# Kernel tuning notes

Measured on AMD Instinct MI355X. Metric: run time of the kernel, lower is better.

Reference implementation:

```python
import jax, jax.numpy as jnp
import numpy as np

B, CIN, COUT, K, H, W = 8, 256, 256, 3, 64, 64
STRIDE, PAD, DIL, DG = 1, 1, 1, 1
K2 = K * K


def _conv2d(x, w, b):
    out = jax.lax.conv_general_dilated(
        x, w, (STRIDE, STRIDE), [(PAD, PAD), (PAD, PAD)],
        rhs_dilation=(DIL, DIL),
        dimension_numbers=('NCHW', 'OIHW', 'NCHW'))
    return out + b[None, :, None, None]


def _deform_conv2d(x, offset, mask, weight, bias):
    # torchvision.ops.deform_conv2d semantics (DCNv2, bilinear, zero outside).
    Bn, Cin, Hin, Win = x.shape
    O = weight.shape[0]
    dg, Cg = DG, Cin // DG
    Ho, Wo = offset.shape[2], offset.shape[3]
    # offset channel layout: [dg, K2, (dy,dx)] interleaved per kernel point
    off = offset.reshape(Bn, dg, K2, 2, Ho, Wo)
    dy, dx = off[:, :, :, 0], off[:, :, :, 1]
    m = mask.reshape(Bn, dg, K2, Ho, Wo)
    ky, kx = jnp.meshgrid(jnp.arange(K), jnp.arange(K), indexing='ij')
    ky = ky.reshape(K2).astype(x.dtype)
    kx = kx.reshape(K2).astype(x.dtype)
    base_y = jnp.arange(Ho, dtype=x.dtype) * STRIDE - PAD
    base_x = jnp.arange(Wo, dtype=x.dtype) * STRIDE - PAD
    # sampling positions [B, dg, K2, Ho, Wo]
    py = base_y[None, None, None, :, None] + (ky * DIL)[None, None, :, None, None] + dy
    px = base_x[None, None, None, None, :] + (kx * DIL)[None, None, :, None, None] + dx
    y0 = jnp.floor(py)
    x0 = jnp.floor(px)
    ly, lx = py - y0, px - x0

    xflat = x.reshape(Bn, dg, Cg, Hin * Win)

    def gather_one(xg, idx):
        return jnp.take(xg, idx, axis=1)

    gather = jax.vmap(jax.vmap(gather_one))  # over B, dg

    def corner(yc, xc, wgt):
        valid = (yc >= 0) & (yc <= Hin - 1) & (xc >= 0) & (xc <= Win - 1)
        yi = jnp.clip(yc, 0, Hin - 1).astype(jnp.int32)
        xi = jnp.clip(xc, 0, Win - 1).astype(jnp.int32)
        idx = (yi * Win + xi).reshape(Bn, dg, K2 * Ho * Wo)
        v = gather(xflat, idx).reshape(Bn, dg, Cg, K2, Ho, Wo)
        w = jnp.where(valid, wgt, jnp.zeros_like(wgt))
        return v * w[:, :, None]  # broadcast over Cg

    sampled = (corner(y0, x0, (1 - ly) * (1 - lx))
               + corner(y0, x0 + 1, (1 - ly) * lx)
               + corner(y0 + 1, x0, ly * (1 - lx))
               + corner(y0 + 1, x0 + 1, ly * lx))
    sampled = sampled * m[:, :, None]  # modulation mask
    wk = weight.reshape(O, dg, Cg, K2)
    out = jnp.einsum('ogck,bgckhw->bohw', wk, sampled)
    return out + bias[None, :, None, None]


def reference(x, weight, bias, w_off, b_off):
    om = _conv2d(x, w_off, b_off)  # [B, 3*dg*K2, H, W]
    n = DG * K2
    o1, o2, mask = om[:, :n], om[:, n:2 * n], om[:, 2 * n:]
    offset = jnp.concatenate([o1, o2], axis=1)
    mask = jax.nn.sigmoid(mask)
    return _deform_conv2d(x, offset, mask, weight, bias)


def setup_inputs():
    key = jax.random.key(0)
    k1, k2, k3, k4, k5 = jax.random.split(key, 5)
    fan_in = CIN * K2
    bound = 1.0 / np.sqrt(fan_in).astype(np.float32)
    x = jax.random.normal(k1, (B, CIN, H, W), dtype=jnp.float32)
    weight = jax.random.uniform(k2, (COUT, CIN, K, K), minval=-bound, maxval=bound, dtype=jnp.float32)
    bias = jax.random.uniform(k3, (COUT,), minval=-bound, maxval=bound, dtype=jnp.float32)
    # small random offset-conv params (zero init in the source is degenerate)
    w_off = jax.random.normal(k4, (3 * K2 * DG, CIN, K, K), dtype=jnp.float32) * 0.01
    b_off = jax.random.normal(k5, (3 * K2 * DG,), dtype=jnp.float32) * 0.01
    return {"x": x, "weight": weight, "bias": bias, "w_off": w_off, "b_off": b_off}
```

## Files before the change

### kernel.cpp

```cpp
#include <hip/hip_runtime.h>
#include <hip/hip_bf16.h>
#include <stdint.h>

typedef short bf16x8 __attribute__((ext_vector_type(8)));
typedef float f32x4  __attribute__((ext_vector_type(4)));

#define NB   8
#define NC   256
#define NO   256
#define HH   64
#define WW   64
#define NPIX 4096
#define KTOT 2304
#define NKC  72

#define XN_OFF  0u
#define XN_SZ   (NB*NPIX*NC*2u)
#define WP_OFF  (XN_OFF + XN_SZ)
#define WP_SZ   (KTOT*NO*2u)
#define WPO_OFF (WP_OFF + WP_SZ)
#define WPO_SZ  (KTOT*32u*2u)
#define OM_OFF  (WPO_OFF + WPO_SZ)
#define OM_SZ   (NB*NPIX*32u*4u)
#define PY_OFF  (OM_OFF + OM_SZ)
#define CO_SZ   (NB*9u*NPIX*4u)
#define PX_OFF  (PY_OFF + CO_SZ)
#define MK_OFF  (PX_OFF + CO_SZ)

__device__ __forceinline__ float b2f(short s) {
    union { unsigned u; float f; } z; z.u = ((unsigned)(unsigned short)s) << 16; return z.f;
}
__device__ __forceinline__ short f2b(float f) {
    __hip_bfloat16 h = __float2bfloat16(f);
    short s; __builtin_memcpy(&s, &h, 2); return s;
}

__global__ void pack_x(const float* __restrict__ x, unsigned short* __restrict__ xn) {
    __shared__ float tile[64][65];
    int blk = blockIdx.x;
    int pt = blk & 63, ct = (blk >> 6) & 3, b = blk >> 8;
    int t = threadIdx.x;
    int pi = t & 63, ci0 = t >> 6;
    const float* src = x + ((size_t)(b*NC + ct*64))*NPIX + (size_t)pt*64;
#pragma unroll
    for (int j = 0; j < 16; ++j)
        tile[ci0 + 4*j][pi] = src[(size_t)(ci0 + 4*j)*NPIX + pi];
    __syncthreads();
    int c = t & 63, pj0 = t >> 6;
    unsigned short* dst = xn + ((size_t)b*NPIX + (size_t)pt*64)*NC + ct*64;
#pragma unroll
    for (int j = 0; j < 16; ++j) {
        int pj = pj0 + 4*j;
        dst[(size_t)pj*NC + c] = (unsigned short)f2b(tile[c][pj]);
    }
}

__global__ void pack_w(const float* __restrict__ weight, unsigned short* __restrict__ wp) {
    int idx = blockIdx.x*256 + threadIdx.x;
    int e = idx & 7, l = (idx >> 3) & 63, nt = (idx >> 9) & 15, kc = idx >> 13;
    int k  = kc*32 + 8*(l >> 4) + e;
    int k2 = k >> 8, c = k & 255;
    int ky = k2 / 3, kx = k2 - 3*ky;
    int o  = nt*16 + (l & 15);
    float v = weight[(size_t)(o*NC + c)*9 + ky*3 + kx];
    wp[idx] = (unsigned short)f2b(v);
}

__global__ void pack_wo(const float* __restrict__ w_off, unsigned short* __restrict__ wpo) {
    int idx = blockIdx.x*256 + threadIdx.x;
    int e = idx & 7, l = (idx >> 3) & 63, nt = (idx >> 9) & 1, kc = idx >> 10;
    int k  = kc*32 + 8*(l >> 4) + e;
    int k2 = k >> 8, c = k & 255;
    int ky = k2 / 3, kx = k2 - 3*ky;
    int n  = nt*16 + (l & 15);
    float v = (n < 27) ? w_off[(size_t)(n*NC + c)*9 + ky*3 + kx] : 0.0f;
    wpo[idx] = (unsigned short)f2b(v);
}

__launch_bounds__(256, 2)
__global__ void off_conv(const unsigned short* __restrict__ xn,
                         const unsigned short* __restrict__ wpo,
                         float* __restrict__ om) {
    int bid = blockIdx.x;
    int lid = (bid & 7)*64 + (bid >> 3);
    int mt = lid & 63, b = lid >> 6;
    int t = threadIdx.x, wv = t >> 6, l = t & 63, g = l >> 4;
    int pix = mt*64 + wv*16 + (l & 15);
    int y = pix >> 6, xx = pix & 63;
    f32x4 acc0 = {0.f,0.f,0.f,0.f}, acc1 = {0.f,0.f,0.f,0.f};
    const char* xc = (const char*)(xn + (size_t)b*NPIX*NC);
    const bf16x8* wpf = (const bf16x8*)wpo;
    const bf16x8 zero8 = {0,0,0,0,0,0,0,0};

    auto aaddr = [&](int kc)->const char* {
        int k2 = kc >> 3, cc = kc & 7;
        int ky = k2 / 3, kx = k2 - 3*ky;
        int sy = y + ky - 1, sx = xx + kx - 1;
        int cs = min(max(sy,0),HH-1)*WW + min(max(sx,0),WW-1);
        return xc + ((size_t)cs*NC + cc*32 + g*8)*2;
    };
    auto avalid = [&](int kc)->bool {
        int k2 = kc >> 3;
        int ky = k2 / 3, kx = k2 - 3*ky;
        int sy = y + ky - 1, sx = xx + kx - 1;
        return (sy>=0)&(sy<HH)&(sx>=0)&(sx<WW);
    };

    bf16x8 a_c = *(const bf16x8*)aaddr(0);
    bf16x8 w0c = wpf[l], w1c = wpf[64 + l];
    bool v_c = avalid(0);
#pragma unroll
    for (int kc = 0; kc < NKC; ++kc) {
        int kn = (kc < NKC-1) ? kc+1 : kc;
        bf16x8 a_n = *(const bf16x8*)aaddr(kn);
        bf16x8 w0n = wpf[(size_t)(kn*2)*64 + l];
        bf16x8 w1n = wpf[(size_t)(kn*2+1)*64 + l];
        bool v_n = avalid(kn);
        bf16x8 au = v_c ? a_c : zero8;
        acc0 = __builtin_amdgcn_mfma_f32_16x16x32_bf16(au, w0c, acc0, 0, 0, 0);
        acc1 = __builtin_amdgcn_mfma_f32_16x16x32_bf16(au, w1c, acc1, 0, 0, 0);
        a_c = a_n; w0c = w0n; w1c = w1n; v_c = v_n;
    }
#pragma unroll
    for (int r = 0; r < 4; ++r) {
        int pm = mt*64 + wv*16 + 4*g + r;
        om[((size_t)b*NPIX + pm)*32 +      (l & 15)] = acc0[r];
        om[((size_t)b*NPIX + pm)*32 + 16 + (l & 15)] = acc1[r];
    }
}

__global__ void coords_k(const float* __restrict__ om, const float* __restrict__ b_off,
                         float* __restrict__ py, float* __restrict__ px,
                         float* __restrict__ mk) {
    int idx = blockIdx.x*256 + threadIdx.x;
    if (idx >= NB*9*NPIX) return;
    int pix = idx & 4095;
    int k   = (idx >> 12) % 9;
    int b   = idx / (9*NPIX);
    const float* omp = om + ((size_t)b*NPIX + pix)*32;
    float dy = omp[2*k]     + b_off[2*k];
    float dx = omp[2*k + 1] + b_off[2*k + 1];
    float m  = omp[18 + k]  + b_off[18 + k];
    float yy = (float)(pix >> 6) - 1.0f + (float)(k / 3) + dy;
    float xv = (float)(pix & 63) - 1.0f + (float)(k % 3) + dx;
    py[idx] = yy;
    px[idx] = xv;
    mk[idx] = 1.0f / (1.0f + __expf(-m));
}

__launch_bounds__(256, 2)
__global__ void dcn_main(const unsigned short* __restrict__ xn,
                         const unsigned short* __restrict__ wpack,
                         const float* __restrict__ pyA,
                         const float* __restrict__ pxA,
                         const float* __restrict__ mkA,
                         const float* __restrict__ bias,
                         float* __restrict__ out) {
    __shared__ unsigned short lds[2][4096];
    int bid = blockIdx.x;
    int lid = (bid & 7)*64 + (bid >> 3);
    int nh  = lid & 1;
    int mtg = lid >> 1;
    int mt = mtg & 31, b = mtg >> 5;
    int t = threadIdx.x, wv = t >> 6, l = t & 63, g = l >> 4;
    int pix0 = mt*128 + wv*32 + (l & 15);

    f32x4 acc[2][8];
#pragma unroll
    for (int f = 0; f < 2; ++f)
#pragma unroll
        for (int nt = 0; nt < 8; ++nt) acc[f][nt] = f32x4{0.f,0.f,0.f,0.f};

    const char* xc = (const char*)(xn + (size_t)b*NPIX*NC);
    const unsigned short* wpb = wpack + nh*4096 + wv*1024 + l*8;

    float cw[2][4];  const char* bp[2][4];
    float ncw[2][4]; const char* nbp[2][4];
    float npy[2], npx[2], nm[2];

    auto coord_compute = [&](float py, float px, float m, float* cwf, const char** bpf) {
        float y0f = floorf(py), x0f = floorf(px);
        float ly = py - y0f, lx = px - x0f;
        int iy0 = (int)y0f, ix0 = (int)x0f;
        int iy1 = iy0 + 1,  ix1 = ix0 + 1;
        bool vy0 = (iy0 >= 0) & (iy0 < HH);
        bool vy1 = (iy1 >= 0) & (iy1 < HH);
        bool vx0 = (ix0 >= 0) & (ix0 < WW);
        bool vx1 = (ix1 >= 0) & (ix1 < WW);
        float wy0 = (1.f - ly) * m, wy1 = ly * m;
        cwf[0] = (vy0 & vx0) ? wy0 * (1.f - lx) : 0.f;
        cwf[1] = (vy0 & vx1) ? wy0 * lx         : 0.f;
        cwf[2] = (vy1 & vx0) ? wy1 * (1.f - lx) : 0.f;
        cwf[3] = (vy1 & vx1) ? wy1 * lx         : 0.f;
        int cy0 = min(max(iy0,0),HH-1), cy1 = min(max(iy1,0),HH-1);
        int cx0 = min(max(ix0,0),WW-1), cx1 = min(max(ix1,0),WW-1);
        bpf[0] = xc + ((size_t)(cy0*WW + cx0)*NC + g*8)*2;
        bpf[1] = xc + ((size_t)(cy0*WW + cx1)*NC + g*8)*2;
        bpf[2] = xc + ((size_t)(cy1*WW + cx0)*NC + g*8)*2;
        bpf[3] = xc + ((size_t)(cy1*WW + cx1)*NC + g*8)*2;
    };

#define STAGEW(bi, kcs) do {                                                           \
        const unsigned short* _gs = wpb + (size_t)(kcs)*8192;                          \
        _Pragma("unroll")                                                              \
        for (int _i = 0; _i < 2; ++_i) {                                               \
            __builtin_amdgcn_global_load_lds(                                          \
                (const __attribute__((address_space(1))) unsigned int*)(_gs + _i*512), \
                (__attribute__((address_space(3))) unsigned int*)(&lds[bi][wv*1024 + _i*512]), \
                16, 0, 0);                                                             \
        }                                                                              \
    } while (0)

#pragma unroll
    for (int f = 0; f < 2; ++f) {
        int ci = ((b*9) << 12) + pix0 + f*16;
        coord_compute(pyA[ci], pxA[ci], mkA[ci], cw[f], bp[f]);
    }
    bf16x8 cur[2][4], nxt[2][4];
#pragma unroll
    for (int f = 0; f < 2; ++f)
#pragma unroll
        for (int c = 0; c < 4; ++c)
            cur[f][c] = *(const bf16x8*)bp[f][c];
    STAGEW(0, 0);
    __syncthreads();

    for (int k2 = 0; k2 < 9; ++k2) {
        int k2n = (k2 < 8) ? k2 + 1 : 8;
#pragma unroll
        for (int cc = 0; cc < 8; ++cc) {
            int kc = k2*8 + cc;
            if (kc < NKC-1) STAGEW((kc+1) & 1, kc+1);
            if (cc == 2) {
#pragma unroll
                for (int f = 0; f < 2; ++f) {
                    int ci = ((b*9 + k2n) << 12) + pix0 + f*16;
                    npy[f] = pyA[ci]; npx[f] = pxA[ci]; nm[f] = mkA[ci];
                }
            }
            if (cc == 5) {
#pragma unroll
                for (int f = 0; f < 2; ++f)
                    coord_compute(npy[f], npx[f], nm[f], ncw[f], nbp[f]);
            }
#pragma unroll
            for (int f = 0; f < 2; ++f)
#pragma unroll
                for (int c = 0; c < 4; ++c)
                    nxt[f][c] = (cc < 7) ? *(const bf16x8*)(bp[f][c] + (cc+1)*64)
                                         : *(const bf16x8*)(nbp[f][c]);
            bf16x8 af[2];
#pragma unroll
            for (int f = 0; f < 2; ++f) {
#pragma unroll
                for (int e = 0; e < 8; ++e) {
                    float v = cw[f][0]*b2f(cur[f][0][e]) + cw[f][1]*b2f(cur[f][1][e])
                            + cw[f][2]*b2f(cur[f][2][e]) + cw[f][3]*b2f(cur[f][3][e]);
                    af[f][e] = f2b(v);
                }
            }
            const bf16x8* bl = (const bf16x8*)&lds[kc & 1][0];
#pragma unroll
            for (int nt = 0; nt < 8; ++nt) {
                bf16x8 wf = bl[nt*64 + l];
                acc[0][nt] = __builtin_amdgcn_mfma_f32_16x16x32_bf16(af[0], wf, acc[0][nt], 0, 0, 0);
                acc[1][nt] = __builtin_amdgcn_mfma_f32_16x16x32_bf16(af[1], wf, acc[1][nt], 0, 0, 0);
            }
            __syncthreads();
#pragma unroll
            for (int f = 0; f < 2; ++f)
#pragma unroll
                for (int c = 0; c < 4; ++c)
                    cur[f][c] = nxt[f][c];
            if (cc == 7) {
#pragma unroll
                for (int f = 0; f < 2; ++f)
#pragma unroll
                    for (int c = 0; c < 4; ++c) { cw[f][c] = ncw[f][c]; bp[f][c] = nbp[f][c]; }
            }
        }
    }
#undef STAGEW

#pragma unroll
    for (int f = 0; f < 2; ++f)
#pragma unroll
        for (int nt = 0; nt < 8; ++nt) {
            int o = nh*128 + nt*16 + (l & 15);
            float bv = bias[o];
            f32x4 r = acc[f][nt] + bv;
            *(f32x4*)(out + ((size_t)(b*NO + o))*NPIX + (mt*128 + wv*32 + f*16 + 4*g)) = r;
        }
}

extern "C" void kernel_launch(void* const* d_in, const int* in_sizes, int n_in,
                              void* d_out, int out_size, void* d_ws, size_t ws_size,
                              hipStream_t stream) {
    const float* x      = (const float*)d_in[0];
    const float* weight = (const float*)d_in[1];
    const float* bias   = (const float*)d_in[2];
    const float* w_off  = (const float*)d_in[3];
    const float* b_off  = (const float*)d_in[4];
    float* out = (float*)d_out;
    char* ws = (char*)d_ws;

    unsigned short* xn  = (unsigned short*)(ws + XN_OFF);
    unsigned short* wp  = (unsigned short*)(ws + WP_OFF);
    unsigned short* wpo = (unsigned short*)(ws + WPO_OFF);
    float* om = (float*)(ws + OM_OFF);
    float* py = (float*)(ws + PY_OFF);
    float* px = (float*)(ws + PX_OFF);
    float* mk = (float*)(ws + MK_OFF);

    pack_x  <<<2048, 256, 0, stream>>>(x, xn);
    pack_w  <<<KTOT*NO/256,  256, 0, stream>>>(weight, wp);
    pack_wo <<<KTOT*32/256,  256, 0, stream>>>(w_off, wpo);
    off_conv<<<512, 256, 0, stream>>>(xn, wpo, om);
    coords_k<<<NB*9*NPIX/256, 256, 0, stream>>>(om, b_off, py, px, mk);
    dcn_main<<<512, 256, 0, stream>>>(xn, wp, py, px, mk, bias, out);
}
```

Baseline: 265.5 us.

## Vectorize pack_x, deepen off_conv prefetch, triple-buffer dcn_main with smaller tiles

pack_x now uses 16-byte vector loads and stores instead of scalar accesses. off_conv moves to 128-thread blocks with a three-stage register prefetch. dcn_main halves its per-block pixel tile and doubles the grid. It adds a third LDS weight buffer and replaces the per-step __syncthreads with explicit vmcnt waits and raw barriers, aiming to overlap global loads with MFMA work and raise occupancy. The hand-tuned waitcnt counts are fragile and could race if the compiler reorders loads, and smaller tiles reduce weight reuse per block.

```diff
diff --git a/kernel.cpp b/kernel.cpp
--- a/kernel.cpp
+++ b/kernel.cpp
@@ -40,18 +40,26 @@
     int blk = blockIdx.x;
     int pt = blk & 63, ct = (blk >> 6) & 3, b = blk >> 8;
     int t = threadIdx.x;
-    int pi = t & 63, ci0 = t >> 6;
+    int ci = t >> 4, p4 = (t & 15) * 4;
     const float* src = x + ((size_t)(b*NC + ct*64))*NPIX + (size_t)pt*64;
 #pragma unroll
-    for (int j = 0; j < 16; ++j)
-        tile[ci0 + 4*j][pi] = src[(size_t)(ci0 + 4*j)*NPIX + pi];
+    for (int j = 0; j < 4; ++j) {
+        f32x4 v = *(const f32x4*)(src + (size_t)(ci + 16*j)*NPIX + p4);
+        tile[ci + 16*j][p4+0] = v[0];
+        tile[ci + 16*j][p4+1] = v[1];
+        tile[ci + 16*j][p4+2] = v[2];
+        tile[ci + 16*j][p4+3] = v[3];
+    }
     __syncthreads();
-    int c = t & 63, pj0 = t >> 6;
-    unsigned short* dst = xn + ((size_t)b*NPIX + (size_t)pt*64)*NC + ct*64;
-#pragma unroll
-    for (int j = 0; j < 16; ++j) {
-        int pj = pj0 + 4*j;
-        dst[(size_t)pj*NC + c] = (unsigned short)f2b(tile[c][pj]);
+    int c8 = (t & 7) * 8, pj0 = t >> 3;
+    unsigned short* dst = xn + ((size_t)b*NPIX + (size_t)pt*64)*NC + ct*64 + c8;
+#pragma unroll
+    for (int j = 0; j < 2; ++j) {
+        int pj = pj0 + 32*j;
+        bf16x8 o;
+#pragma unroll
+        for (int e = 0; e < 8; ++e) o[e] = f2b(tile[c8 + e][pj]);
+        *(bf16x8*)(dst + (size_t)pj*NC) = o;
     }
 }
 
@@ -77,15 +85,14 @@
     wpo[idx] = (unsigned short)f2b(v);
 }
 
-__launch_bounds__(256, 2)
+__launch_bounds__(128, 4)
 __global__ void off_conv(const unsigned short* __restrict__ xn,
                          const unsigned short* __restrict__ wpo,
                          float* __restrict__ om) {
     int bid = blockIdx.x;
-    int lid = (bid & 7)*64 + (bid >> 3);
-    int mt = lid & 63, b = lid >> 6;
+    int b = bid & 7, mt = bid >> 3;
     int t = threadIdx.x, wv = t >> 6, l = t & 63, g = l >> 4;
-    int pix = mt*64 + wv*16 + (l & 15);
+    int pix = mt*32 + wv*16 + (l & 15);
     int y = pix >> 6, xx = pix & 63;
     f32x4 acc0 = {0.f,0.f,0.f,0.f}, acc1 = {0.f,0.f,0.f,0.f};
     const char* xc = (const char*)(xn + (size_t)b*NPIX*NC);
@@ -106,24 +113,32 @@
         return (sy>=0)&(sy<HH)&(sx>=0)&(sx<WW);
     };
 
-    bf16x8 a_c = *(const bf16x8*)aaddr(0);
-    bf16x8 w0c = wpf[l], w1c = wpf[64 + l];
-    bool v_c = avalid(0);
+    bf16x8 a[3], w0[3], w1[3];
+    bool v[3];
+#pragma unroll
+    for (int s = 0; s < 3; ++s) {
+        a[s]  = *(const bf16x8*)aaddr(s);
+        w0[s] = wpf[(size_t)(s*2)*64 + l];
+        w1[s] = wpf[(size_t)(s*2+1)*64 + l];
+        v[s]  = avalid(s);
+    }
 #pragma unroll
     for (int kc = 0; kc < NKC; ++kc) {
-        int kn = (kc < NKC-1) ? kc+1 : kc;
-        bf16x8 a_n = *(const bf16x8*)aaddr(kn);
-        bf16x8 w0n = wpf[(size_t)(kn*2)*64 + l];
-        bf16x8 w1n = wpf[(size_t)(kn*2+1)*64 + l];
-        bool v_n = avalid(kn);
-        bf16x8 au = v_c ? a_c : zero8;
-        acc0 = __builtin_amdgcn_mfma_f32_16x16x32_bf16(au, w0c, acc0, 0, 0, 0);
-        acc1 = __builtin_amdgcn_mfma_f32_16x16x32_bf16(au, w1c, acc1, 0, 0, 0);
-        a_c = a_n; w0c = w0n; w1c = w1n; v_c = v_n;
+        int s = kc % 3;
+        bf16x8 au = v[s] ? a[s] : zero8;
+        acc0 = __builtin_amdgcn_mfma_f32_16x16x32_bf16(au, w0[s], acc0, 0, 0, 0);
+        acc1 = __builtin_amdgcn_mfma_f32_16x16x32_bf16(au, w1[s], acc1, 0, 0, 0);
+        int kp = kc + 3;
+        if (kp < NKC) {
+            a[s]  = *(const bf16x8*)aaddr(kp);
+            w0[s] = wpf[(size_t)(kp*2)*64 + l];
+            w1[s] = wpf[(size_t)(kp*2+1)*64 + l];
+            v[s]  = avalid(kp);
+        }
     }
 #pragma unroll
     for (int r = 0; r < 4; ++r) {
-        int pm = mt*64 + wv*16 + 4*g + r;
+        int pm = mt*32 + wv*16 + 4*g + r;
         om[((size_t)b*NPIX + pm)*32 +      (l & 15)] = acc0[r];
         om[((size_t)b*NPIX + pm)*32 + 16 + (l & 15)] = acc1[r];
     }
@@ -148,7 +163,7 @@
     mk[idx] = 1.0f / (1.0f + __expf(-m));
 }
 
-__launch_bounds__(256, 2)
+__launch_bounds__(256, 4)
 __global__ void dcn_main(const unsigned short* __restrict__ xn,
                          const unsigned short* __restrict__ wpack,
                          const float* __restrict__ pyA,
@@ -156,27 +171,24 @@
                          const float* __restrict__ mkA,
                          const float* __restrict__ bias,
                          float* __restrict__ out) {
-    __shared__ unsigned short lds[2][4096];
+    __shared__ unsigned short lds[3][4096];
     int bid = blockIdx.x;
-    int lid = (bid & 7)*64 + (bid >> 3);
-    int nh  = lid & 1;
-    int mtg = lid >> 1;
-    int mt = mtg & 31, b = mtg >> 5;
+    int b   = bid & 7;
+    int loc = bid >> 3;
+    int mt  = loc >> 1, nh = loc & 1;
     int t = threadIdx.x, wv = t >> 6, l = t & 63, g = l >> 4;
-    int pix0 = mt*128 + wv*32 + (l & 15);
-
-    f32x4 acc[2][8];
-#pragma unroll
-    for (int f = 0; f < 2; ++f)
-#pragma unroll
-        for (int nt = 0; nt < 8; ++nt) acc[f][nt] = f32x4{0.f,0.f,0.f,0.f};
+    int pix0 = mt*64 + wv*16 + (l & 15);
+
+    f32x4 acc[8];
+#pragma unroll
+    for (int i = 0; i < 8; ++i) acc[i] = f32x4{0.f,0.f,0.f,0.f};
 
     const char* xc = (const char*)(xn + (size_t)b*NPIX*NC);
     const unsigned short* wpb = wpack + nh*4096 + wv*1024 + l*8;
 
-    float cw[2][4];  const char* bp[2][4];
-    float ncw[2][4]; const char* nbp[2][4];
-    float npy[2], npx[2], nm[2];
+    float cw[4], ncw[4];
+    const char *bp[4], *nbp[4];
+    float npy, npx, nm;
 
     auto coord_compute = [&](float py, float px, float m, float* cwf, const char** bpf) {
         float y0f = floorf(py), x0f = floorf(px);
@@ -200,97 +212,95 @@
         bpf[3] = xc + ((size_t)(cy1*WW + cx1)*NC + g*8)*2;
     };
 
-#define STAGEW(bi, kcs) do {                                                           \
+#define STAGEW(bufi, kcs) do {                                                         \
         const unsigned short* _gs = wpb + (size_t)(kcs)*8192;                          \
+        unsigned short* _ld = &lds[0][0] + (size_t)(bufi)*4096 + wv*1024;              \
         _Pragma("unroll")                                                              \
         for (int _i = 0; _i < 2; ++_i) {                                               \
             __builtin_amdgcn_global_load_lds(                                          \
                 (const __attribute__((address_space(1))) unsigned int*)(_gs + _i*512), \
-                (__attribute__((address_space(3))) unsigned int*)(&lds[bi][wv*1024 + _i*512]), \
+                (__attribute__((address_space(3))) unsigned int*)(_ld + _i*512),       \
                 16, 0, 0);                                                             \
         }                                                                              \
     } while (0)
 
-#pragma unroll
-    for (int f = 0; f < 2; ++f) {
-        int ci = ((b*9) << 12) + pix0 + f*16;
-        coord_compute(pyA[ci], pxA[ci], mkA[ci], cw[f], bp[f]);
-    }
-    bf16x8 cur[2][4], nxt[2][4];
-#pragma unroll
-    for (int f = 0; f < 2; ++f)
-#pragma unroll
-        for (int c = 0; c < 4; ++c)
-            cur[f][c] = *(const bf16x8*)bp[f][c];
+    {
+        int ci = (b*9 << 12) + pix0;
+        coord_compute(pyA[ci], pxA[ci], mkA[ci], cw, bp);
+    }
+    bf16x8 cA[4], cB[4];
+#pragma unroll
+    for (int c = 0; c < 4; ++c) cA[c] = *(const bf16x8*)bp[c];
     STAGEW(0, 0);
-    __syncthreads();
-
+#pragma unroll
+    for (int c = 0; c < 4; ++c) cB[c] = *(const bf16x8*)(bp[c] + 64);
+    STAGEW(1, 1);
+    __builtin_amdgcn_sched_barrier(0);
+    asm volatile("s_waitcnt vmcnt(6)" ::: "memory");
+    __builtin_amdgcn_s_barrier();
+    __builtin_amdgcn_sched_barrier(0);
+
+    int rb = 0, sb = 2;
     for (int k2 = 0; k2 < 9; ++k2) {
         int k2n = (k2 < 8) ? k2 + 1 : 8;
 #pragma unroll
         for (int cc = 0; cc < 8; ++cc) {
             int kc = k2*8 + cc;
-            if (kc < NKC-1) STAGEW((kc+1) & 1, kc+1);
-            if (cc == 2) {
-#pragma unroll
-                for (int f = 0; f < 2; ++f) {
-                    int ci = ((b*9 + k2n) << 12) + pix0 + f*16;
-                    npy[f] = pyA[ci]; npx[f] = pxA[ci]; nm[f] = mkA[ci];
-                }
+            if (cc == 1) {
+                int ci = ((b*9 + k2n) << 12) + pix0;
+                npy = pyA[ci]; npx = pxA[ci]; nm = mkA[ci];
             }
-            if (cc == 5) {
-#pragma unroll
-                for (int f = 0; f < 2; ++f)
-                    coord_compute(npy[f], npx[f], nm[f], ncw[f], nbp[f]);
+            bf16x8 af;
+#pragma unroll
+            for (int e = 0; e < 8; ++e) {
+                const bf16x8* S = (cc & 1) ? cB : cA;
+                float vv = cw[0]*b2f(S[0][e]) + cw[1]*b2f(S[1][e])
+                         + cw[2]*b2f(S[2][e]) + cw[3]*b2f(S[3][e]);
+                af[e] = f2b(vv);
             }
-#pragma unroll
-            for (int f = 0; f < 2; ++f)
+            const bf16x8* bl = (const bf16x8*)(&lds[0][0] + (size_t)rb*4096);
+#pragma unroll
+            for (int nt = 0; nt < 8; ++nt)
+                acc[nt] = __builtin_amdgcn_mfma_f32_16x16x32_bf16(af, bl[nt*64 + l], acc[nt], 0, 0, 0);
+            if (cc == 4) coord_compute(npy, npx, nm, ncw, nbp);
+            if (cc <= 5) {
 #pragma unroll
                 for (int c = 0; c < 4; ++c)
-                    nxt[f][c] = (cc < 7) ? *(const bf16x8*)(bp[f][c] + (cc+1)*64)
-                                         : *(const bf16x8*)(nbp[f][c]);
-            bf16x8 af[2];
-#pragma unroll
-            for (int f = 0; f < 2; ++f) {
-#pragma unroll
-                for (int e = 0; e < 8; ++e) {
-                    float v = cw[f][0]*b2f(cur[f][0][e]) + cw[f][1]*b2f(cur[f][1][e])
-                            + cw[f][2]*b2f(cur[f][2][e]) + cw[f][3]*b2f(cur[f][3][e]);
-                    af[f][e] = f2b(v);
-                }
+                    ((cc & 1) ? cB : cA)[c] = *(const bf16x8*)(bp[c] + (cc+2)*64);
+            } else if (cc == 6) {
+#pragma unroll
+                for (int c = 0; c < 4; ++c) cA[c] = *(const bf16x8*)(nbp[c]);
+            } else {
+#pragma unroll
+                for (int c = 0; c < 4; ++c) cB[c] = *(const bf16x8*)(nbp[c] + 64);
             }
-            const bf16x8* bl = (const bf16x8*)&lds[kc & 1][0];
-#pragma unroll
-            for (int nt = 0; nt < 8; ++nt) {
-                bf16x8 wf = bl[nt*64 + l];
-                acc[0][nt] = __builtin_amdgcn_mfma_f32_16x16x32_bf16(af[0], wf, acc[0][nt], 0, 0, 0);
-                acc[1][nt] = __builtin_amdgcn_mfma_f32_16x16x32_bf16(af[1], wf, acc[1][nt], 0, 0, 0);
+            int kcs = kc + 2; if (kcs > NKC-1) kcs = NKC-1;
+            STAGEW(sb, kcs);
+            if (cc == 7) {
+#pragma unroll
+                for (int c = 0; c < 4; ++c) { cw[c] = ncw[c]; bp[c] = nbp[c]; }
             }
-            __syncthreads();
-#pragma unroll
-            for (int f = 0; f < 2; ++f)
-#pragma unroll
-                for (int c = 0; c < 4; ++c)
-                    cur[f][c] = nxt[f][c];
-            if (cc == 7) {
-#pragma unroll
-                for (int f = 0; f < 2; ++f)
-#pragma unroll
-                    for (int c = 0; c < 4; ++c) { cw[f][c] = ncw[f][c]; bp[f][c] = nbp[f][c]; }
-            }
+            sb = rb; rb = (rb == 2) ? 0 : rb + 1;
+            __builtin_amdgcn_sched_barrier(0);
+            if (cc == 1) asm volatile("s_waitcnt vmcnt(9)" ::: "memory");
+            else         asm volatile("s_waitcnt vmcnt(6)" ::: "memory");
+            __builtin_amdgcn_s_barrier();
+            __builtin_amdgcn_sched_barrier(0);
         }
     }
 #undef STAGEW
-
-#pragma unroll
-    for (int f = 0; f < 2; ++f)
-#pragma unroll
-        for (int nt = 0; nt < 8; ++nt) {
-            int o = nh*128 + nt*16 + (l & 15);
-            float bv = bias[o];
-            f32x4 r = acc[f][nt] + bv;
-            *(f32x4*)(out + ((size_t)(b*NO + o))*NPIX + (mt*128 + wv*32 + f*16 + 4*g)) = r;
-        }
+    asm volatile("" :: "v"(cA[0]), "v"(cA[1]), "v"(cA[2]), "v"(cA[3]),
+                       "v"(cB[0]), "v"(cB[1]), "v"(cB[2]), "v"(cB[3]));
+    asm volatile("s_waitcnt vmcnt(0)" ::: "memory");
+
+    int pmbase = mt*64 + wv*16 + 4*g;
+#pragma unroll
+    for (int nt = 0; nt < 8; ++nt) {
+        int o = nh*128 + nt*16 + (l & 15);
+        float bv = bias[o];
+        f32x4 r = acc[nt] + bv;
+        *(f32x4*)(out + ((size_t)(b*NO + o))*NPIX + pmbase) = r;
+    }
 }
 
 extern "C" void kernel_launch(void* const* d_in, const int* in_sizes, int n_in,
@@ -315,7 +325,7 @@
     pack_x  <<<2048, 256, 0, stream>>>(x, xn);
     pack_w  <<<KTOT*NO/256,  256, 0, stream>>>(weight, wp);
     pack_wo <<<KTOT*32/256,  256, 0, stream>>>(w_off, wpo);
-    off_conv<<<512, 256, 0, stream>>>(xn, wpo, om);
+    off_conv<<<1024, 128, 0, stream>>>(xn, wpo, om);
     coords_k<<<NB*9*NPIX/256, 256, 0, stream>>>(om, b_off, py, px, mk);
-    dcn_main<<<512, 256, 0, stream>>>(xn, wp, py, px, mk, bias, out);
-}
+    dcn_main<<<1024, 256, 0, stream>>>(xn, wp, py, px, mk, bias, out);
+}
```

Measured after the change: 273.7 us. 1.03x slower.

## Restage DCN weights in larger LDS phases, vectorize packing, and use packed bf16 blend

Applied to the files above, without the earlier changes.

The main deformable kernel now stages four k-chunks of weights per phase into a 64KB double-buffered LDS area. This cuts barriers from 72 to 18. It also drops the software-prefetch register pipeline for the gathered corners in favour of direct loads inside each phase. Bilinear blending now works on 32-bit pairs and converts with v_cvt_pk_bf16_f32. pack_x uses vectorized loads and stores, and off_conv drops manual prefetch while raising its occupancy target and changing the block-to-batch mapping. The larger LDS footprint may limit occupancy, and removing the prefetch may expose gather latency.

```diff
diff --git a/kernel.cpp b/kernel.cpp
--- a/kernel.cpp
+++ b/kernel.cpp
@@ -4,6 +4,7 @@
 
 typedef short bf16x8 __attribute__((ext_vector_type(8)));
 typedef float f32x4  __attribute__((ext_vector_type(4)));
+typedef int   i32x4  __attribute__((ext_vector_type(4)));
 
 #define NB   8
 #define NC   256
@@ -34,24 +35,53 @@
     __hip_bfloat16 h = __float2bfloat16(f);
     short s; __builtin_memcpy(&s, &h, 2); return s;
 }
+__device__ __forceinline__ float dw_lo(int u) {
+    union { int i; float f; } z; z.i = u << 16; return z.f;
+}
+__device__ __forceinline__ float dw_hi(int u) {
+    union { int i; float f; } z; z.i = u & 0xFFFF0000; return z.f;
+}
+
+__device__ __forceinline__ bf16x8 blend4(bf16x8 c0, bf16x8 c1, bf16x8 c2, bf16x8 c3,
+                                         float w0, float w1, float w2, float w3) {
+    union U { bf16x8 s; i32x4 i; } u0, u1, u2, u3, r;
+    u0.s = c0; u1.s = c1; u2.s = c2; u3.s = c3;
+#pragma unroll
+    for (int d = 0; d < 4; ++d) {
+        float lo = w0*dw_lo(u0.i[d]) + w1*dw_lo(u1.i[d]) + w2*dw_lo(u2.i[d]) + w3*dw_lo(u3.i[d]);
+        float hi = w0*dw_hi(u0.i[d]) + w1*dw_hi(u1.i[d]) + w2*dw_hi(u2.i[d]) + w3*dw_hi(u3.i[d]);
+        int pk;
+        asm("v_cvt_pk_bf16_f32 %0, %1, %2" : "=v"(pk) : "v"(lo), "v"(hi));
+        r.i[d] = pk;
+    }
+    return r.s;
+}
 
 __global__ void pack_x(const float* __restrict__ x, unsigned short* __restrict__ xn) {
     __shared__ float tile[64][65];
     int blk = blockIdx.x;
     int pt = blk & 63, ct = (blk >> 6) & 3, b = blk >> 8;
     int t = threadIdx.x;
-    int pi = t & 63, ci0 = t >> 6;
+    int ci = t >> 4, p4 = (t & 15) * 4;
     const float* src = x + ((size_t)(b*NC + ct*64))*NPIX + (size_t)pt*64;
 #pragma unroll
-    for (int j = 0; j < 16; ++j)
-        tile[ci0 + 4*j][pi] = src[(size_t)(ci0 + 4*j)*NPIX + pi];
+    for (int j = 0; j < 4; ++j) {
+        f32x4 v = *(const f32x4*)(src + (size_t)(ci + 16*j)*NPIX + p4);
+        tile[ci + 16*j][p4+0] = v[0];
+        tile[ci + 16*j][p4+1] = v[1];
+        tile[ci + 16*j][p4+2] = v[2];
+        tile[ci + 16*j][p4+3] = v[3];
+    }
     __syncthreads();
-    int c = t & 63, pj0 = t >> 6;
-    unsigned short* dst = xn + ((size_t)b*NPIX + (size_t)pt*64)*NC + ct*64;
-#pragma unroll
-    for (int j = 0; j < 16; ++j) {
-        int pj = pj0 + 4*j;
-        dst[(size_t)pj*NC + c] = (unsigned short)f2b(tile[c][pj]);
+    int c8 = (t & 7) * 8, pj0 = t >> 3;
+    unsigned short* dst = xn + ((size_t)b*NPIX + (size_t)pt*64)*NC + ct*64 + c8;
+#pragma unroll
+    for (int j = 0; j < 2; ++j) {
+        int pj = pj0 + 32*j;
+        bf16x8 o;
+#pragma unroll
+        for (int e = 0; e < 8; ++e) o[e] = f2b(tile[c8 + e][pj]);
+        *(bf16x8*)(dst + (size_t)pj*NC) = o;
     }
 }
 
@@ -77,13 +107,12 @@
     wpo[idx] = (unsigned short)f2b(v);
 }
 
-__launch_bounds__(256, 2)
+__launch_bounds__(256, 4)
 __global__ void off_conv(const unsigned short* __restrict__ xn,
                          const unsigned short* __restrict__ wpo,
                          float* __restrict__ om) {
     int bid = blockIdx.x;
-    int lid = (bid & 7)*64 + (bid >> 3);
-    int mt = lid & 63, b = lid >> 6;
+    int b = bid & 7, mt = bid >> 3;
     int t = threadIdx.x, wv = t >> 6, l = t & 63, g = l >> 4;
     int pix = mt*64 + wv*16 + (l & 15);
     int y = pix >> 6, xx = pix & 63;
@@ -91,35 +120,19 @@
     const char* xc = (const char*)(xn + (size_t)b*NPIX*NC);
     const bf16x8* wpf = (const bf16x8*)wpo;
     const bf16x8 zero8 = {0,0,0,0,0,0,0,0};
-
-    auto aaddr = [&](int kc)->const char* {
+#pragma unroll
+    for (int kc = 0; kc < NKC; ++kc) {
         int k2 = kc >> 3, cc = kc & 7;
         int ky = k2 / 3, kx = k2 - 3*ky;
         int sy = y + ky - 1, sx = xx + kx - 1;
+        bool valid = (sy>=0)&(sy<HH)&(sx>=0)&(sx<WW);
         int cs = min(max(sy,0),HH-1)*WW + min(max(sx,0),WW-1);
-        return xc + ((size_t)cs*NC + cc*32 + g*8)*2;
-    };
-    auto avalid = [&](int kc)->bool {
-        int k2 = kc >> 3;
-        int ky = k2 / 3, kx = k2 - 3*ky;
-        int sy = y + ky - 1, sx = xx + kx - 1;
-        return (sy>=0)&(sy<HH)&(sx>=0)&(sx<WW);
-    };
-
-    bf16x8 a_c = *(const bf16x8*)aaddr(0);
-    bf16x8 w0c = wpf[l], w1c = wpf[64 + l];
-    bool v_c = avalid(0);
-#pragma unroll
-    for (int kc = 0; kc < NKC; ++kc) {
-        int kn = (kc < NKC-1) ? kc+1 : kc;
-        bf16x8 a_n = *(const bf16x8*)aaddr(kn);
-        bf16x8 w0n = wpf[(size_t)(kn*2)*64 + l];
-        bf16x8 w1n = wpf[(size_t)(kn*2+1)*64 + l];
-        bool v_n = avalid(kn);
-        bf16x8 au = v_c ? a_c : zero8;
-        acc0 = __builtin_amdgcn_mfma_f32_16x16x32_bf16(au, w0c, acc0, 0, 0, 0);
-        acc1 = __builtin_amdgcn_mfma_f32_16x16x32_bf16(au, w1c, acc1, 0, 0, 0);
-        a_c = a_n; w0c = w0n; w1c = w1n; v_c = v_n;
+        bf16x8 a = *(const bf16x8*)(xc + ((size_t)cs*NC + cc*32 + g*8)*2);
+        bf16x8 w0 = wpf[(size_t)(kc*2  )*64 + l];
+        bf16x8 w1 = wpf[(size_t)(kc*2+1)*64 + l];
+        bf16x8 au = valid ? a : zero8;
+        acc0 = __builtin_amdgcn_mfma_f32_16x16x32_bf16(au, w0, acc0, 0, 0, 0);
+        acc1 = __builtin_amdgcn_mfma_f32_16x16x32_bf16(au, w1, acc1, 0, 0, 0);
     }
 #pragma unroll
     for (int r = 0; r < 4; ++r) {
@@ -156,12 +169,11 @@
                          const float* __restrict__ mkA,
                          const float* __restrict__ bias,
                          float* __restrict__ out) {
-    __shared__ unsigned short lds[2][4096];
+    __shared__ char lds[2][32768];
     int bid = blockIdx.x;
-    int lid = (bid & 7)*64 + (bid >> 3);
-    int nh  = lid & 1;
-    int mtg = lid >> 1;
-    int mt = mtg & 31, b = mtg >> 5;
+    int b  = bid & 7;
+    int u  = bid >> 3;
+    int nh = u & 1, mt = u >> 1;
     int t = threadIdx.x, wv = t >> 6, l = t & 63, g = l >> 4;
     int pix0 = mt*128 + wv*32 + (l & 15);
 
@@ -172,11 +184,6 @@
         for (int nt = 0; nt < 8; ++nt) acc[f][nt] = f32x4{0.f,0.f,0.f,0.f};
 
     const char* xc = (const char*)(xn + (size_t)b*NPIX*NC);
-    const unsigned short* wpb = wpack + nh*4096 + wv*1024 + l*8;
-
-    float cw[2][4];  const char* bp[2][4];
-    float ncw[2][4]; const char* nbp[2][4];
-    float npy[2], npx[2], nm[2];
 
     auto coord_compute = [&](float py, float px, float m, float* cwf, const char** bpf) {
         float y0f = floorf(py), x0f = floorf(px);
@@ -200,88 +207,58 @@
         bpf[3] = xc + ((size_t)(cy1*WW + cx1)*NC + g*8)*2;
     };
 
-#define STAGEW(bi, kcs) do {                                                           \
-        const unsigned short* _gs = wpb + (size_t)(kcs)*8192;                          \
-        _Pragma("unroll")                                                              \
-        for (int _i = 0; _i < 2; ++_i) {                                               \
-            __builtin_amdgcn_global_load_lds(                                          \
-                (const __attribute__((address_space(1))) unsigned int*)(_gs + _i*512), \
-                (__attribute__((address_space(3))) unsigned int*)(&lds[bi][wv*1024 + _i*512]), \
-                16, 0, 0);                                                             \
-        }                                                                              \
-    } while (0)
-
-#pragma unroll
-    for (int f = 0; f < 2; ++f) {
-        int ci = ((b*9) << 12) + pix0 + f*16;
-        coord_compute(pyA[ci], pxA[ci], mkA[ci], cw[f], bp[f]);
-    }
-    bf16x8 cur[2][4], nxt[2][4];
-#pragma unroll
-    for (int f = 0; f < 2; ++f)
-#pragma unroll
-        for (int c = 0; c < 4; ++c)
-            cur[f][c] = *(const bf16x8*)bp[f][c];
-    STAGEW(0, 0);
+    auto stage = [&](int buf, int ph) {
+        int k2 = ph >> 1, h = ph & 1;
+        int kcp = k2*8 + h*4 + wv;
+        const unsigned short* gs = wpack + ((size_t)(kcp*16 + nh*8))*512 + l*8;
+        char* ld = &lds[buf][wv*8192];
+#pragma unroll
+        for (int i = 0; i < 8; ++i) {
+            __builtin_amdgcn_global_load_lds(
+                (const __attribute__((address_space(1))) unsigned int*)(gs + i*512),
+                (__attribute__((address_space(3))) unsigned int*)(ld + i*1024),
+                16, 0, 0);
+        }
+    };
+
+    stage(0, 0);
     __syncthreads();
 
-    for (int k2 = 0; k2 < 9; ++k2) {
-        int k2n = (k2 < 8) ? k2 + 1 : 8;
-#pragma unroll
-        for (int cc = 0; cc < 8; ++cc) {
-            int kc = k2*8 + cc;
-            if (kc < NKC-1) STAGEW((kc+1) & 1, kc+1);
-            if (cc == 2) {
-#pragma unroll
-                for (int f = 0; f < 2; ++f) {
-                    int ci = ((b*9 + k2n) << 12) + pix0 + f*16;
-                    npy[f] = pyA[ci]; npx[f] = pxA[ci]; nm[f] = mkA[ci];
-                }
+    for (int ph = 0; ph < 18; ++ph) {
+        int buf = ph & 1;
+        if (ph < 17) stage(buf ^ 1, ph + 1);
+        int k2 = ph >> 1, h = ph & 1;
+
+        float cw[2][4]; const char* bp[2][4];
+#pragma unroll
+        for (int f = 0; f < 2; ++f) {
+            int ci = ((b*9 + k2) << 12) + pix0 + f*16;
+            coord_compute(pyA[ci], pxA[ci], mkA[ci], cw[f], bp[f]);
+        }
+#pragma unroll
+        for (int s = 0; s < 4; ++s) {
+            int cb = (h*4 + s)*64;
+            bf16x8 af[2];
+#pragma unroll
+            for (int f = 0; f < 2; ++f) {
+                bf16x8 c0 = *(const bf16x8*)(bp[f][0] + cb);
+                bf16x8 c1 = *(const bf16x8*)(bp[f][1] + cb);
+                bf16x8 c2 = *(const bf16x8*)(bp[f][2] + cb);
+                bf16x8 c3 = *(const bf16x8*)(bp[f][3] + cb);
+                af[f] = blend4(c0, c1, c2, c3, cw[f][0], cw[f][1], cw[f][2], cw[f][3]);
             }
-            if (cc == 5) {
-#pragma unroll
-                for (int f = 0; f < 2; ++f)
-                    coord_compute(npy[f], npx[f], nm[f], ncw[f], nbp[f]);
-            }
-#pragma unroll
-            for (int f = 0; f < 2; ++f)
-#pragma unroll
-                for (int c = 0; c < 4; ++c)
-                    nxt[f][c] = (cc < 7) ? *(const bf16x8*)(bp[f][c] + (cc+1)*64)
-                                         : *(const bf16x8*)(nbp[f][c]);
-            bf16x8 af[2];
-#pragma unroll
-            for (int f = 0; f < 2; ++f) {
-#pragma unroll
-                for (int e = 0; e < 8; ++e) {
-                    float v = cw[f][0]*b2f(cur[f][0][e]) + cw[f][1]*b2f(cur[f][1][e])
-                            + cw[f][2]*b2f(cur[f][2][e]) + cw[f][3]*b2f(cur[f][3][e]);
-                    af[f][e] = f2b(v);
-                }
-            }
-            const bf16x8* bl = (const bf16x8*)&lds[kc & 1][0];
+            const char* blp = &lds[buf][s*8192];
 #pragma unroll
             for (int nt = 0; nt < 8; ++nt) {
-                bf16x8 wf = bl[nt*64 + l];
+                bf16x8 wf = *(const bf16x8*)(blp + nt*1024 + l*16);
                 acc[0][nt] = __builtin_amdgcn_mfma_f32_16x16x32_bf16(af[0], wf, acc[0][nt], 0, 0, 0);
                 acc[1][nt] = __builtin_amdgcn_mfma_f32_16x16x32_bf16(af[1], wf, acc[1][nt], 0, 0, 0);
             }
-            __syncthreads();
-#pragma unroll
-            for (int f = 0; f < 2; ++f)
-#pragma unroll
-                for (int c = 0; c < 4; ++c)
-                    cur[f][c] = nxt[f][c];
-            if (cc == 7) {
-#pragma unroll
-                for (int f = 0; f < 2; ++f)
-#pragma unroll
-                    for (int c = 0; c < 4; ++c) { cw[f][c] = ncw[f][c]; bp[f][c] = nbp[f][c]; }
-            }
-        }
-    }
-#undef STAGEW
-
+        }
+        __syncthreads();
+    }
+
+    int pmbase = mt*128 + wv*32 + 4*g;
 #pragma unroll
     for (int f = 0; f < 2; ++f)
 #pragma unroll
@@ -289,7 +266,7 @@
             int o = nh*128 + nt*16 + (l & 15);
             float bv = bias[o];
             f32x4 r = acc[f][nt] + bv;
-            *(f32x4*)(out + ((size_t)(b*NO + o))*NPIX + (mt*128 + wv*32 + f*16 + 4*g)) = r;
+            *(f32x4*)(out + ((size_t)(b*NO + o))*NPIX + pmbase + f*16) = r;
         }
 }
 
```

Result: no change. 264.0 us (-0.5%).
